# Kernel tuning notes

Measured on AMD Instinct MI355X. Metric: run time of the kernel, lower is better.

## Reference

```python
import jax, jax.numpy as jnp
import numpy as np

B, S, HID = 2, 2048, 4096
H, P, N, G, K = 128, 64, 128, 8, 4      # heads, head_dim, ssm_state, groups, conv kernel
INTER = H * P                           # 8192
CONV_DIM = INTER + 2 * G * N            # 10240
CHUNK = 128
EPS = 1e-5
DT_MIN, DT_MAX = 0.0, 100.0


def setup_inputs() -> dict:
    key = jax.random.key(0)
    ks = jax.random.split(key, 4)
    proj = INTER + CONV_DIM + H
    return {
        "x": jax.random.normal(ks[0], (B, S, HID), jnp.float32),
        "in_proj_w": jax.random.normal(ks[1], (proj, HID), jnp.float32) * 0.02,
        "conv_w": jax.random.normal(ks[2], (CONV_DIM, 1, K), jnp.float32) * 0.2,
        "conv_b": jnp.zeros((CONV_DIM,), jnp.float32),
        "dt_bias": jnp.ones((H,), jnp.float32),
        "A_log": jnp.log(jnp.arange(1, H + 1, dtype=jnp.float32)),
        "D": jnp.ones((H,), jnp.float32),
        "norm_w": jnp.ones((INTER,), jnp.float32),
        "out_proj_w": jax.random.normal(ks[3], (HID, INTER), jnp.float32) * 0.02,
    }


def _segsum(a):
    # a: (..., c) -> (..., c, c); [i, j] = sum_{k=j+1..i} a[k] for i >= j, else -inf
    c = a.shape[-1]
    s = jnp.cumsum(a, axis=-1)
    diff = s[..., :, None] - s[..., None, :]
    mask = jnp.tril(jnp.ones((c, c), dtype=bool))
    return jnp.where(mask, diff, -jnp.inf)


def reference(x, in_proj_w, conv_w, conv_b, dt_bias, A_log, D, norm_w, out_proj_w):
    b, s, _ = x.shape
    proj = jnp.einsum('bsd,ed->bse', x, in_proj_w)
    gate = proj[..., :INTER]
    hBC = proj[..., INTER:INTER + CONV_DIM]
    dt = proj[..., INTER + CONV_DIM:]                       # (b, s, H)

    # depthwise causal conv1d + silu
    xc = jnp.transpose(hBC, (0, 2, 1))                      # (b, conv_dim, s)
    xc = jax.lax.conv_general_dilated(xc, conv_w, (1,), [(K - 1, 0)],
                                      dimension_numbers=('NCH', 'OIH', 'NCH'),
                                      feature_group_count=CONV_DIM)
    xc = xc + conv_b[None, :, None]
    hBC = jax.nn.silu(jnp.transpose(xc, (0, 2, 1)))

    hs = hBC[..., :INTER].reshape(b, s, H, P)
    Bm = hBC[..., INTER:INTER + G * N].reshape(b, s, G, N)
    Cm = hBC[..., INTER + G * N:].reshape(b, s, G, N)

    A = -jnp.exp(A_log)                                     # (H,)
    dt = jnp.clip(jax.nn.softplus(dt + dt_bias), DT_MIN, DT_MAX)

    rep = H // G
    Bh = jnp.repeat(Bm, rep, axis=2)                        # (b, s, H, N)
    Ch = jnp.repeat(Cm, rep, axis=2)

    nc = s // CHUNK
    xch = (hs * dt[..., None]).reshape(b, nc, CHUNK, H, P)  # dt-scaled input, chunked
    Bc = Bh.reshape(b, nc, CHUNK, H, N)
    Cc = Ch.reshape(b, nc, CHUNK, H, N)
    A_dt = (dt * A).reshape(b, nc, CHUNK, H).transpose(0, 3, 1, 2)  # (b, H, nc, c)
    A_cum = jnp.cumsum(A_dt, axis=-1)

    # intra-chunk (diagonal) contribution
    L = jnp.exp(_segsum(A_dt))                              # (b, H, nc, c, c)
    Y_diag = jnp.einsum('bzlhn,bzshn,bhzls,bzshp->bzlhp', Cc, Bc, L, xch)

    # per-chunk final states
    decay_states = jnp.exp(A_cum[..., -1:] - A_cum)         # (b, H, nc, c)
    states = jnp.einsum('bzlhn,bhzl,bzlhp->bzhpn', Bc, decay_states, xch)

    # inter-chunk recurrence (initial state = 0)
    states_p = jnp.concatenate([jnp.zeros_like(states[:, :1]), states], axis=1)  # (b, nc+1, H, P, N)
    A_last = jnp.pad(A_cum[..., -1], ((0, 0), (0, 0), (1, 0)))                   # (b, H, nc+1)
    decay_chunk = jnp.exp(_segsum(A_last))                                        # (b, H, nc+1, nc+1)
    new_states = jnp.einsum('bhzc,bchpn->bzhpn', decay_chunk, states_p)
    prev = new_states[:, :-1]                                # state entering each chunk

    Y_off = jnp.einsum('bzlhn,bzhpn,bhzl->bzlhp', Cc, prev, jnp.exp(A_cum))
    Y = (Y_diag + Y_off).reshape(b, s, H, P) + hs * D[None, None, :, None]
    y = Y.reshape(b, s, INTER)

    # gated grouped RMSNorm (norm_before_gate=False)
    g = y * jax.nn.silu(gate)
    gg = g.reshape(b, s, G, INTER // G)
    var = jnp.mean(gg * gg, axis=-1, keepdims=True)
    gg = gg * jax.lax.rsqrt(var + EPS)
    out = gg.reshape(b, s, INTER) * norm_w

    return jnp.einsum('bsi,oi->bso', out, out_proj_w)
```

## Files before the change

kernel.cpp:

```cpp
#include <hip/hip_runtime.h>
#include <hip/hip_bf16.h>
#include <cstdint>
#include <cstddef>

#define DEVI __device__ __forceinline__

#define BB 2
#define S_LEN 2048
#define HID_DIM 4096
#define NH 128
#define PD 64
#define NS 128
#define NG 8
#define INTER 8192
#define CONVD 10240
#define PROJ 18560
#define PROJP 18688
#define NC 16
#define BS 4096
#define GN 1024

using short8 = __attribute__((ext_vector_type(8))) short;
using short4v = __attribute__((ext_vector_type(4))) short;
using f32x4  = __attribute__((ext_vector_type(4))) float;
using bf16x8 = __attribute__((ext_vector_type(8))) __bf16;

DEVI float bf2f(short u) {
  union { unsigned int i; float f; } v;
  v.i = ((unsigned int)(unsigned short)u) << 16;
  return v.f;
}
DEVI short f2bf(float f) {
  union { float ff; unsigned int i; } v; v.ff = f;
  unsigned int x = v.i;
  return (short)((x + 0x7fffu + ((x >> 16) & 1u)) >> 16);
}
DEVI f32x4 mfma16(short8 a, short8 b, f32x4 c) {
  return __builtin_amdgcn_mfma_f32_16x16x32_bf16(
      __builtin_bit_cast(bf16x8, a), __builtin_bit_cast(bf16x8, b), c, 0, 0, 0);
}
DEVI void gl_lds16(const short* g, short* l) {
  __builtin_amdgcn_global_load_lds(
      (const __attribute__((address_space(1))) void*)g,
      (__attribute__((address_space(3))) void*)l, 16, 0, 0);
}
DEVI float sigmoidf_(float x) { return 1.f / (1.f + __expf(-x)); }

__global__ __launch_bounds__(256) void cvt_f32_bf16_k(const float* __restrict__ in,
                                                      short* __restrict__ out, size_t n) {
  size_t i = ((size_t)blockIdx.x * 256 + threadIdx.x) * 8;
  if (i + 8 > n) return;
  float4 a = *(const float4*)(in + i);
  float4 b = *(const float4*)(in + i + 4);
  short8 o;
  o[0] = f2bf(a.x); o[1] = f2bf(a.y); o[2] = f2bf(a.z); o[3] = f2bf(a.w);
  o[4] = f2bf(b.x); o[5] = f2bf(b.y); o[6] = f2bf(b.z); o[7] = f2bf(b.w);
  *(short8*)(out + i) = o;
}


#define STG(ISB, BUF, KH, TILE) do { \
  const short* _src = (ISB) ? Bt : A; \
  const int _r0 = (ISB) ? n0 : m0; \
  short* _lb = lds_ + ((ISB) ? 32768 : 0) + ((BUF)*2+(KH))*8192; \
  const int _kt = (TILE)*64 + (KH)*32; \
  { int _row = (wid*2)*16 + srow; int _sl = sps ^ ((_row>>1)&3); \
    gl_lds16(_src + (size_t)(_r0+_row)*K + _kt + _sl*8, _lb + (wid*2)*512); } \
  { int _row = (wid*2+1)*16 + srow; int _sl = sps ^ ((_row>>1)&3); \
    gl_lds16(_src + (size_t)(_r0+_row)*K + _kt + _sl*8, _lb + (wid*2+1)*512); } \
} while(0)

#define NOPS ((void)0)
#define VM6 asm volatile("s_waitcnt vmcnt(6)" ::: "memory")
#define VM0 asm volatile("s_waitcnt vmcnt(0)" ::: "memory")

#define PH(BUF, KH, MIH, DOB, STGS, VMW) do { \
  _Pragma("unroll") \
  for (int _m = 0; _m < 4; ++_m) { \
    int _row = wr*128 + ((MIH)*4+_m)*16 + fr; \
    af[_m] = *(const short8*)(lds_ + ((BUF)*2+(KH))*8192 + _row*32 + ((slot ^ ((_row>>1)&3))<<3)); \
  } \
  if (DOB) { \
    _Pragma("unroll") \
    for (int _n = 0; _n < 4; ++_n) { \
      int _row = wc*64 + _n*16 + fr; \
      bf_[_n] = *(const short8*)(lds_ + 32768 + ((BUF)*2+(KH))*8192 + _row*32 + ((slot ^ ((_row>>1)&3))<<3)); \
    } \
  } \
  STGS; VMW; \
  __builtin_amdgcn_s_barrier(); \
  asm volatile("s_waitcnt lgkmcnt(0)" ::: "memory"); \
  __builtin_amdgcn_sched_barrier(0); \
  __builtin_amdgcn_s_setprio(1); \
  _Pragma("unroll") \
  for (int _m = 0; _m < 4; ++_m) \
    _Pragma("unroll") \
    for (int _n = 0; _n < 4; ++_n) \
      acc[(MIH)*4+_m][_n] = mfma16(af[_m], bf_[_n], acc[(MIH)*4+_m][_n]); \
  __builtin_amdgcn_s_setprio(0); \
  __builtin_amdgcn_s_barrier(); \
} while(0)

template<int CB16>
__global__ __launch_bounds__(512, 2) void gemm256_k(const short* __restrict__ A,
                                                    const short* __restrict__ Bt,
                                                    void* __restrict__ Cout,
                                                    int Nstride, int K, int ntn) {
  __shared__ short lds_[65536];
  const int tid = threadIdx.x, wid = tid >> 6, lane = tid & 63;
  const int nwg = gridDim.x, orig = blockIdx.x;
  const int swz = (orig & 7) * (nwg >> 3) + (orig >> 3);
  const int per_group = ntn << 3;
  const int group = swz / per_group;
  const int rem = swz - group * per_group;
  const int m0 = (group * 8 + (rem & 7)) * 256;
  const int n0 = (rem >> 3) * 256;
  const int wr = wid >> 2, wc = wid & 3;
  const int fr = lane & 15, slot = lane >> 4;
  const int srow = lane >> 2, sps = lane & 3;

  f32x4 acc[8][4] = {};
  short8 af[4], bf_[4];
  const int NT = K >> 6;

  STG(1, 0, 0, 0); STG(0, 0, 0, 0); STG(1, 0, 1, 0); STG(0, 0, 1, 0);
  asm volatile("s_waitcnt vmcnt(4)" ::: "memory");
  STG(1, 1, 0, 1); STG(0, 1, 0, 1); STG(1, 1, 1, 1);
  asm volatile("s_waitcnt vmcnt(6)" ::: "memory");
  __builtin_amdgcn_s_barrier();

  for (int i = 0; i < (NT >> 1) - 1; ++i) {
    const int t = 2 * i;
    PH(0, 0, 0, 1, STG(0, 1, 1, t + 1), NOPS);
    PH(0, 0, 1, 0, STG(1, 0, 0, t + 2), NOPS);
    PH(0, 1, 0, 1, STG(0, 0, 0, t + 2), NOPS);
    PH(0, 1, 1, 0, STG(1, 0, 1, t + 2), VM6);
    PH(1, 0, 0, 1, STG(0, 0, 1, t + 2), NOPS);
    PH(1, 0, 1, 0, STG(1, 1, 0, t + 3), NOPS);
    PH(1, 1, 0, 1, STG(0, 1, 0, t + 3), NOPS);
    PH(1, 1, 1, 0, STG(1, 1, 1, t + 3), VM6);
  }
  PH(0, 0, 0, 1, STG(0, 1, 1, NT - 1), NOPS);
  PH(0, 0, 1, 0, NOPS, NOPS);
  PH(0, 1, 0, 1, NOPS, NOPS);
  PH(0, 1, 1, 0, NOPS, VM0);
  PH(1, 0, 0, 1, NOPS, NOPS);
  PH(1, 0, 1, 0, NOPS, NOPS);
  PH(1, 1, 0, 1, NOPS, NOPS);
  PH(1, 1, 1, 0, NOPS, NOPS);

  const int er = (lane >> 4) * 4, ec = lane & 15;
  if (CB16) {
    short* C = (short*)Cout;
#pragma unroll
    for (int mi = 0; mi < 8; ++mi)
#pragma unroll
      for (int j = 0; j < 4; ++j) {
        size_t base = (size_t)(m0 + wr * 128 + mi * 16 + er + j) * Nstride + n0 + wc * 64 + ec;
#pragma unroll
        for (int ni = 0; ni < 4; ++ni) C[base + ni * 16] = f2bf(acc[mi][ni][j]);
      }
  } else {
    float* C = (float*)Cout;
#pragma unroll
    for (int mi = 0; mi < 8; ++mi)
#pragma unroll
      for (int j = 0; j < 4; ++j) {
        size_t base = (size_t)(m0 + wr * 128 + mi * 16 + er + j) * Nstride + n0 + wc * 64 + ec;
#pragma unroll
        for (int ni = 0; ni < 4; ++ni) C[base + ni * 16] = acc[mi][ni][j];
      }
  }
}

__global__ __launch_bounds__(256) void conv_silu_k(const short* __restrict__ projb,
                                                   const float* __restrict__ convw,
                                                   const float* __restrict__ convb,
                                                   short* __restrict__ hbc) {
  const int c = blockIdx.x * 256 + threadIdx.x;
  const int s0 = blockIdx.y * 256;
  const int b = blockIdx.z;
  const size_t rb = (size_t)b * S_LEN;
  const float* wp = convw + (size_t)c * 4;
  const float w0 = wp[0], w1 = wp[1], w2 = wp[2], w3 = wp[3];
  const float bias = convb[c];
  const short* pcol = projb + INTER + c;
  float x1 = 0.f, x2 = 0.f, x3 = 0.f;
  if (s0 > 0) {
    x3 = bf2f(pcol[(rb + s0 - 3) * PROJP]);
    x2 = bf2f(pcol[(rb + s0 - 2) * PROJP]);
    x1 = bf2f(pcol[(rb + s0 - 1) * PROJP]);
  }
  for (int s = s0; s < s0 + 256; ++s) {
    float v = bf2f(pcol[(rb + s) * PROJP]);
    float acc = bias + w0 * x3 + w1 * x2 + w2 * x1 + w3 * v;
    float o = acc * sigmoidf_(acc);
    hbc[(rb + s) * CONVD + c] = f2bf(o);
    x3 = x2; x2 = x1; x1 = v;
  }
}

__global__ __launch_bounds__(128) void acum_k(const short* __restrict__ projb,
                                              const float* __restrict__ dt_bias,
                                              const float* __restrict__ A_log,
                                              float* __restrict__ dtT,
                                              float* __restrict__ acum) {
  const int l = threadIdx.x;
  const int z = blockIdx.x, h = blockIdx.y, b = blockIdx.z;
  const float A = -__expf(A_log[h]);
  __shared__ float sv[128];
  const int r = b * S_LEN + z * 128 + l;
  float xv = bf2f(projb[(size_t)r * PROJP + INTER + CONVD + h]) + dt_bias[h];
  float sp = (xv > 20.f) ? xv : log1pf(__expf(xv));
  sp = fminf(fmaxf(sp, 0.f), 100.f);
  const size_t base = ((size_t)(b * NH + h)) * S_LEN + z * 128;
  dtT[base + l] = sp;
  sv[l] = sp * A;
  __syncthreads();
  for (int off = 1; off < 128; off <<= 1) {
    float t = (l >= off) ? sv[l - off] : 0.f;
    __syncthreads();
    sv[l] += t;
    __syncthreads();
  }
  acum[base + l] = sv[l];
}

__global__ __launch_bounds__(512) void states_k(const short* __restrict__ hbc,
                                                const float* __restrict__ dtT,
                                                const float* __restrict__ acum,
                                                float* __restrict__ states) {
  __shared__ short sB[128 * 128];
  __shared__ short sxdt[64 * 128];
  __shared__ float sac[128];
  const int tid = threadIdx.x, wid = tid >> 6, lane = tid & 63;
  const int g = blockIdx.x, z = blockIdx.y, b = blockIdx.z;
  const size_t srow0 = (size_t)(b * S_LEN + z * 128);
  const short* hrow = hbc + srow0 * CONVD;

  {
    const int n0_ = (lane & 15) * 8;
#pragma unroll
    for (int it = 0; it < 4; ++it) {
      int s = it * 32 + wid * 4 + (lane >> 4);
      gl_lds16(hrow + (size_t)s * CONVD + INTER + g * NS + n0_, sB + (it * 32 + wid * 4) * 128);
    }
  }

  const int fr = lane & 15, fk8 = (lane >> 4) * 8;
  const int er = (lane >> 4) * 4, ec = lane & 15;
  const int nbase = wid * 16;

  for (int hh = 0; hh < 16; ++hh) {
    const int h = g * 16 + hh;
    const float* ac = acum + ((size_t)(b * NH + h)) * S_LEN + z * 128;
    const float* dts = dtT + ((size_t)(b * NH + h)) * S_LEN + z * 128;
    __syncthreads();
    if (tid < 128) sac[tid] = ac[tid];
    {
      int s = tid >> 2, p0 = (tid & 3) * 16;
      float dv = dts[s];
      short8 hv0 = *(const short8*)(hrow + (size_t)s * CONVD + (size_t)h * PD + p0);
      short8 hv1 = *(const short8*)(hrow + (size_t)s * CONVD + (size_t)h * PD + p0 + 8);
#pragma unroll
      for (int j = 0; j < 8; ++j) {
        sxdt[(p0 + j) * 128 + s] = f2bf(bf2f(hv0[j]) * dv);
        sxdt[(p0 + 8 + j) * 128 + s] = f2bf(bf2f(hv1[j]) * dv);
      }
    }
    __syncthreads();
    const float acLast = sac[127];
    f32x4 st[4] = {};
#pragma unroll
    for (int kk = 0; kk < 4; ++kk) {
      short8 a;
#pragma unroll
      for (int j = 0; j < 8; ++j) {
        int l = kk * 32 + fk8 + j;
        float dec = __expf(acLast - sac[l]);
        a[j] = f2bf(bf2f(sB[l * 128 + nbase + fr]) * dec);
      }
#pragma unroll
      for (int ni = 0; ni < 4; ++ni) {
        short8 bv = *(const short8*)(sxdt + (ni * 16 + fr) * 128 + kk * 32 + fk8);
        st[ni] = mfma16(a, bv, st[ni]);
      }
    }
    float* stp = states + (((size_t)(b * NC + z)) * NH + h) * (size_t)(NS * PD);
#pragma unroll
    for (int ni = 0; ni < 4; ++ni)
#pragma unroll
      for (int j = 0; j < 4; ++j)
        stp[(nbase + er + j) * PD + ni * 16 + ec] = st[ni][j];
  }
}

__global__ __launch_bounds__(256) void scan_k(float* __restrict__ states,
                                              const float* __restrict__ acum) {
  const int h = blockIdx.x, b = blockIdx.y;
  const int tid = threadIdx.x;
  float* stp = states + ((size_t)(b * NC * NH) + h) * (size_t)(NS * PD);
  const size_t cst = (size_t)NH * NS * PD;
  const float* ac = acum + ((size_t)(b * NH + h)) * S_LEN;
  float E[32];
#pragma unroll
  for (int i = 0; i < 32; ++i) E[i] = 0.f;
  for (int zz = 0; zz < NC; ++zz) {
    float* sz = stp + (size_t)zz * cst;
    float tmp[32];
#pragma unroll
    for (int i = 0; i < 32; ++i) tmp[i] = sz[i * 256 + tid];
    __syncthreads();
    float dec = __expf(ac[zz * 128 + 127]);
#pragma unroll
    for (int i = 0; i < 32; ++i) {
      int e = i * 256 + tid;
      int n = e >> 6, p = e & 63;
      sz[p * NS + n] = E[i];
      E[i] = dec * E[i] + tmp[i];
    }
    __syncthreads();
  }
}

__global__ __launch_bounds__(512) void yfull_k(const short* __restrict__ hbc,
                                               const short* __restrict__ projb,
                                               const float* __restrict__ dtT,
                                               const float* __restrict__ acum,
                                               const float* __restrict__ states,
                                               const float* __restrict__ Dv,
                                               const float* __restrict__ norm_w,
                                               float* __restrict__ Yg,
                                               short* __restrict__ normed) {
  __shared__ short lds[49152];
  __shared__ float sac[128];
  __shared__ float sScale[128];
  __shared__ float sNW[1024];
  short* sC = lds;
  short* sB = lds + 16384;
  short* sxdt = lds + 16384;
  short* sprev = lds + 16384 + 8192;
  const int tid = threadIdx.x, wid = tid >> 6, lane = tid & 63;
  short* sPw = lds + 32768 + wid * 2048;
  const int g = blockIdx.x, z = blockIdx.y, b = blockIdx.z;
  const size_t srow0 = (size_t)(b * S_LEN + z * 128);
  const short* hrow = hbc + srow0 * CONVD;

  {
    const int n0_ = (lane & 15) * 8;
#pragma unroll
    for (int it = 0; it < 4; ++it) {
      int s = it * 32 + wid * 4 + (lane >> 4);
      gl_lds16(hrow + (size_t)s * CONVD + INTER + GN + g * NS + n0_, sC + (it * 32 + wid * 4) * 128);
      gl_lds16(hrow + (size_t)s * CONVD + INTER + g * NS + n0_, sB + (it * 32 + wid * 4) * 128);
    }
  }
  for (int i = tid; i < 1024; i += 512) sNW[i] = norm_w[g * 1024 + i];
  __syncthreads();

  const int fr = lane & 15, fk8 = (lane >> 4) * 8;
  const int er = (lane >> 4) * 4, ec = lane & 15;
  const int lrow = wid * 16;

  f32x4 sc[8] = {};
#pragma unroll
  for (int kk = 0; kk < 4; ++kk) {
    short8 a = *(const short8*)(sC + (lrow + fr) * 128 + kk * 32 + fk8);
#pragma unroll
    for (int si = 0; si < 8; ++si) {
      short8 bv = *(const short8*)(sB + (si * 16 + fr) * 128 + kk * 32 + fk8);
      sc[si] = mfma16(a, bv, sc[si]);
    }
  }

  float rssq[4] = {0.f, 0.f, 0.f, 0.f};

  for (int hh = 0; hh < 16; ++hh) {
    const int h = g * 16 + hh;
    const float* ac = acum + ((size_t)(b * NH + h)) * S_LEN + z * 128;
    const float* dts = dtT + ((size_t)(b * NH + h)) * S_LEN + z * 128;
    const float* pv = states + (((size_t)(b * NC + z)) * NH + h) * (size_t)(NS * PD);
    __syncthreads();
    if (tid < 128) sac[tid] = ac[tid];
    {
      int s = tid >> 2, p0 = (tid & 3) * 16;
      float dv = dts[s];
      short8 hv0 = *(const short8*)(hrow + (size_t)s * CONVD + (size_t)h * PD + p0);
      short8 hv1 = *(const short8*)(hrow + (size_t)s * CONVD + (size_t)h * PD + p0 + 8);
#pragma unroll
      for (int j = 0; j < 8; ++j) {
        sxdt[(p0 + j) * 128 + s] = f2bf(bf2f(hv0[j]) * dv);
        sxdt[(p0 + 8 + j) * 128 + s] = f2bf(bf2f(hv1[j]) * dv);
      }
    }
#pragma unroll
    for (int it = 0; it < 4; ++it) {
      int e = (it * 512 + tid) * 4;
      float4 v = *(const float4*)(pv + e);
      short4v o;
      o[0] = f2bf(v.x); o[1] = f2bf(v.y); o[2] = f2bf(v.z); o[3] = f2bf(v.w);
      *(short4v*)(sprev + e) = o;
    }
    __syncthreads();

    {
      float acS[8];
#pragma unroll
      for (int si = 0; si < 8; ++si) acS[si] = sac[si * 16 + ec];
#pragma unroll
      for (int j = 0; j < 4; ++j) {
        int lloc = er + j;
        float acl = sac[lrow + lloc];
#pragma unroll
        for (int si = 0; si < 8; ++si) {
          int s = si * 16 + ec;
          float v = (s <= lrow + lloc) ? sc[si][j] * __expf(acl - acS[si]) : 0.f;
          sPw[lloc * 128 + s] = f2bf(v);
        }
      }
    }
    f32x4 yd[4] = {}, yo[4] = {};
#pragma unroll
    for (int kk = 0; kk < 4; ++kk) {
      short8 ap = *(const short8*)(sPw + fr * 128 + kk * 32 + fk8);
      short8 acf = *(const short8*)(sC + (lrow + fr) * 128 + kk * 32 + fk8);
#pragma unroll
      for (int ni = 0; ni < 4; ++ni) {
        short8 bv = *(const short8*)(sxdt + (ni * 16 + fr) * 128 + kk * 32 + fk8);
        yd[ni] = mfma16(ap, bv, yd[ni]);
        short8 bp = *(const short8*)(sprev + (ni * 16 + fr) * 128 + kk * 32 + fk8);
        yo[ni] = mfma16(acf, bp, yo[ni]);
      }
    }
    const float Dh = Dv[h];
#pragma unroll
    for (int j = 0; j < 4; ++j) {
      int l = lrow + er + j;
      float e_ac = __expf(sac[l]);
#pragma unroll
      for (int ni = 0; ni < 4; ++ni) {
        int p = ni * 16 + ec;
        float hs = bf2f(hrow[(size_t)l * CONVD + (size_t)h * PD + p]);
        float y = yd[ni][j] + yo[ni][j] * e_ac + hs * Dh;
        float gate = bf2f(projb[(srow0 + l) * (size_t)PROJP + (size_t)h * PD + p]);
        float gg = y * gate * sigmoidf_(gate);
        Yg[(srow0 + l) * (size_t)INTER + (size_t)h * PD + p] = gg;
        rssq[j] += gg * gg;
      }
    }
  }

#pragma unroll
  for (int j = 0; j < 4; ++j) {
#pragma unroll
    for (int m = 1; m <= 8; m <<= 1) rssq[j] += __shfl_xor(rssq[j], m, 64);
  }
  if (ec == 0) {
#pragma unroll
    for (int j = 0; j < 4; ++j) sScale[lrow + er + j] = rsqrtf(rssq[j] * (1.f / 1024.f) + 1e-5f);
  }
  __syncthreads();

  for (int e = tid * 8; e < 128 * 1024; e += 4096) {
    int row = e >> 10, ch = e & 1023;
    const float* gp = Yg + (srow0 + row) * (size_t)INTER + g * 1024 + ch;
    float4 g0 = *(const float4*)(gp);
    float4 g1 = *(const float4*)(gp + 4);
    float scl = sScale[row];
    short8 o;
    o[0] = f2bf(g0.x * scl * sNW[ch + 0]); o[1] = f2bf(g0.y * scl * sNW[ch + 1]);
    o[2] = f2bf(g0.z * scl * sNW[ch + 2]); o[3] = f2bf(g0.w * scl * sNW[ch + 3]);
    o[4] = f2bf(g1.x * scl * sNW[ch + 4]); o[5] = f2bf(g1.y * scl * sNW[ch + 5]);
    o[6] = f2bf(g1.z * scl * sNW[ch + 6]); o[7] = f2bf(g1.w * scl * sNW[ch + 7]);
    *(short8*)(normed + (srow0 + row) * (size_t)INTER + g * 1024 + ch) = o;
  }
}

extern "C" void kernel_launch(void* const* d_in, const int* in_sizes, int n_in,
                              void* d_out, int out_size, void* d_ws, size_t ws_size,
                              hipStream_t stream) {
  const float* x     = (const float*)d_in[0];
  const float* w1    = (const float*)d_in[1];
  const float* convw = (const float*)d_in[2];
  const float* convb = (const float*)d_in[3];
  const float* dtb   = (const float*)d_in[4];
  const float* alog  = (const float*)d_in[5];
  const float* Dv    = (const float*)d_in[6];
  const float* nw    = (const float*)d_in[7];
  const float* w2    = (const float*)d_in[8];
  float* out = (float*)d_out;

  char* ws = (char*)d_ws;
  size_t off = 0;
  float* dtT = (float*)(ws + off);  off += (size_t)BB * NH * S_LEN * 4;
  float* acum = (float*)(ws + off); off += (size_t)BB * NH * S_LEN * 4;
  short* xb = (short*)(ws + off);   off += (size_t)BS * HID_DIM * 2;
  char* w1region = ws + off;        off += (size_t)PROJP * HID_DIM * 2;
  short* w1b = (short*)w1region;
  short* normed = (short*)w1region;
  short* w2b = (short*)(w1region + (size_t)BS * INTER * 2);
  short* projb = (short*)(ws + off); off += (size_t)BS * PROJP * 2;
  short* hbc = (short*)(ws + off);   off += (size_t)BS * CONVD * 2;
  float* Y = (float*)(ws + off);     off += (size_t)BS * INTER * 4;
  float* states = (float*)(ws + off); off += (size_t)BB * NC * NH * NS * PD * 4;

  const size_t nx = (size_t)BS * HID_DIM;
  const size_t nw1 = (size_t)PROJ * HID_DIM;
  const size_t nw2 = (size_t)HID_DIM * INTER;

  cvt_f32_bf16_k<<<dim3(nx / 2048), 256, 0, stream>>>(x, xb, nx);
  cvt_f32_bf16_k<<<dim3(nw1 / 2048), 256, 0, stream>>>(w1, w1b, nw1);

  gemm256_k<1><<<dim3(16 * 73), 512, 0, stream>>>(xb, w1b, projb, PROJP, HID_DIM, 73);

  cvt_f32_bf16_k<<<dim3(nw2 / 2048), 256, 0, stream>>>(w2, w2b, nw2);

  conv_silu_k<<<dim3(CONVD / 256, S_LEN / 256, BB), 256, 0, stream>>>(projb, convw, convb, hbc);
  acum_k<<<dim3(NC, NH, BB), 128, 0, stream>>>(projb, dtb, alog, dtT, acum);

  states_k<<<dim3(NG, NC, BB), 512, 0, stream>>>(hbc, dtT, acum, states);
  scan_k<<<dim3(NH, BB), 256, 0, stream>>>(states, acum);
  yfull_k<<<dim3(NG, NC, BB), 512, 0, stream>>>(hbc, projb, dtT, acum, states, Dv, nw, Y, normed);

  gemm256_k<0><<<dim3(16 * 16), 512, 0, stream>>>(normed, w2b, out, HID_DIM, INTER, 16);
}
```

Measured before the change: 1.392 ms.

## Restructure SSM state kernels: transposed B tile, bf16 state handoff, padded LDS

Widens the GEMM block swizzle group from 8 to 16 M-tiles to change L2 reuse. The states kernel now folds the decay into the x*dt staging and stores B transposed in LDS, which removes per-element exp and conversion work from the MFMA inner loop. The scan kernel writes the propagated states as bf16 in the layout yfull expects, so yfull can fetch them with direct global-to-LDS loads instead of converting fp32. yfull also packs two bf16 values per 32-bit LDS store and pads its per-wave P rows to reduce bank conflicts. The previous-state operand is now rounded to bf16 in the scan kernel rather than in yfull, and it overwrites the first half of the fp32 state buffer in place.

```diff
diff --git a/kernel.cpp b/kernel.cpp
--- a/kernel.cpp
+++ b/kernel.cpp
@@ -110,11 +110,11 @@
   const int tid = threadIdx.x, wid = tid >> 6, lane = tid & 63;
   const int nwg = gridDim.x, orig = blockIdx.x;
   const int swz = (orig & 7) * (nwg >> 3) + (orig >> 3);
-  const int per_group = ntn << 3;
+  const int per_group = ntn << 4;
   const int group = swz / per_group;
   const int rem = swz - group * per_group;
-  const int m0 = (group * 8 + (rem & 7)) * 256;
-  const int n0 = (rem >> 3) * 256;
+  const int m0 = (group * 16 + (rem & 15)) * 256;
+  const int n0 = (rem >> 4) * 256;
   const int wr = wid >> 2, wc = wid & 3;
   const int fr = lane & 15, slot = lane >> 4;
   const int srow = lane >> 2, sps = lane & 3;
@@ -230,60 +230,63 @@
                                                 const float* __restrict__ dtT,
                                                 const float* __restrict__ acum,
                                                 float* __restrict__ states) {
-  __shared__ short sB[128 * 128];
+  __shared__ short sBT[128 * 128];
   __shared__ short sxdt[64 * 128];
-  __shared__ float sac[128];
   const int tid = threadIdx.x, wid = tid >> 6, lane = tid & 63;
   const int g = blockIdx.x, z = blockIdx.y, b = blockIdx.z;
   const size_t srow0 = (size_t)(b * S_LEN + z * 128);
   const short* hrow = hbc + srow0 * CONVD;
 
   {
-    const int n0_ = (lane & 15) * 8;
-#pragma unroll
-    for (int it = 0; it < 4; ++it) {
-      int s = it * 32 + wid * 4 + (lane >> 4);
-      gl_lds16(hrow + (size_t)s * CONVD + INTER + g * NS + n0_, sB + (it * 32 + wid * 4) * 128);
+    const int l = tid & 127, n0b = (tid >> 7) * 32;
+    const short* src = hrow + (size_t)l * CONVD + INTER + g * NS + n0b;
+    short8 v0 = *(const short8*)(src);
+    short8 v1 = *(const short8*)(src + 8);
+    short8 v2 = *(const short8*)(src + 16);
+    short8 v3 = *(const short8*)(src + 24);
+#pragma unroll
+    for (int j = 0; j < 8; ++j) {
+      sBT[(n0b + j) * 128 + l] = v0[j];
+      sBT[(n0b + 8 + j) * 128 + l] = v1[j];
+      sBT[(n0b + 16 + j) * 128 + l] = v2[j];
+      sBT[(n0b + 24 + j) * 128 + l] = v3[j];
     }
   }
 
   const int fr = lane & 15, fk8 = (lane >> 4) * 8;
   const int er = (lane >> 4) * 4, ec = lane & 15;
-  const int nbase = wid * 16;
+  const int pband = (wid & 3) * 16, nhalf = (wid >> 2) * 64;
+  const int s2 = tid & 63, p0w = (tid >> 6) * 8;
+  unsigned int* sx32 = (unsigned int*)sxdt;
 
   for (int hh = 0; hh < 16; ++hh) {
     const int h = g * 16 + hh;
-    const float* ac = acum + ((size_t)(b * NH + h)) * S_LEN + z * 128;
+    const float* ac_g = acum + ((size_t)(b * NH + h)) * S_LEN + z * 128;
     const float* dts = dtT + ((size_t)(b * NH + h)) * S_LEN + z * 128;
     __syncthreads();
-    if (tid < 128) sac[tid] = ac[tid];
     {
-      int s = tid >> 2, p0 = (tid & 3) * 16;
-      float dv = dts[s];
-      short8 hv0 = *(const short8*)(hrow + (size_t)s * CONVD + (size_t)h * PD + p0);
-      short8 hv1 = *(const short8*)(hrow + (size_t)s * CONVD + (size_t)h * PD + p0 + 8);
+      const float acL = ac_g[127];
+      float dv0 = dts[2 * s2] * __expf(acL - ac_g[2 * s2]);
+      float dv1 = dts[2 * s2 + 1] * __expf(acL - ac_g[2 * s2 + 1]);
+      const short* rsrc = hrow + (size_t)(2 * s2) * CONVD + (size_t)h * PD + p0w;
+      short8 r0 = *(const short8*)(rsrc);
+      short8 r1 = *(const short8*)(rsrc + CONVD);
 #pragma unroll
       for (int j = 0; j < 8; ++j) {
-        sxdt[(p0 + j) * 128 + s] = f2bf(bf2f(hv0[j]) * dv);
-        sxdt[(p0 + 8 + j) * 128 + s] = f2bf(bf2f(hv1[j]) * dv);
-      }
-    }
-    __syncthreads();
-    const float acLast = sac[127];
+        unsigned int lo = (unsigned short)f2bf(bf2f(r0[j]) * dv0);
+        unsigned int hi = (unsigned short)f2bf(bf2f(r1[j]) * dv1);
+        sx32[(p0w + j) * 64 + s2] = lo | (hi << 16);
+      }
+    }
+    __syncthreads();
     f32x4 st[4] = {};
 #pragma unroll
     for (int kk = 0; kk < 4; ++kk) {
-      short8 a;
-#pragma unroll
-      for (int j = 0; j < 8; ++j) {
-        int l = kk * 32 + fk8 + j;
-        float dec = __expf(acLast - sac[l]);
-        a[j] = f2bf(bf2f(sB[l * 128 + nbase + fr]) * dec);
-      }
+      short8 a = *(const short8*)(sxdt + (pband + fr) * 128 + kk * 32 + fk8);
 #pragma unroll
       for (int ni = 0; ni < 4; ++ni) {
-        short8 bv = *(const short8*)(sxdt + (ni * 16 + fr) * 128 + kk * 32 + fk8);
-        st[ni] = mfma16(a, bv, st[ni]);
+        short8 bb = *(const short8*)(sBT + (nhalf + ni * 16 + fr) * 128 + kk * 32 + fk8);
+        st[ni] = mfma16(a, bb, st[ni]);
       }
     }
     float* stp = states + (((size_t)(b * NC + z)) * NH + h) * (size_t)(NS * PD);
@@ -291,7 +294,7 @@
     for (int ni = 0; ni < 4; ++ni)
 #pragma unroll
       for (int j = 0; j < 4; ++j)
-        stp[(nbase + er + j) * PD + ni * 16 + ec] = st[ni][j];
+        stp[(pband + er + j) * NS + nhalf + ni * 16 + ec] = st[ni][j];
   }
 }
 
@@ -305,8 +308,10 @@
   float E[32];
 #pragma unroll
   for (int i = 0; i < 32; ++i) E[i] = 0.f;
+  const int n = tid & 127, pg = tid >> 7;
   for (int zz = 0; zz < NC; ++zz) {
     float* sz = stp + (size_t)zz * cst;
+    short* pvb = (short*)sz;
     float tmp[32];
 #pragma unroll
     for (int i = 0; i < 32; ++i) tmp[i] = sz[i * 256 + tid];
@@ -314,9 +319,8 @@
     float dec = __expf(ac[zz * 128 + 127]);
 #pragma unroll
     for (int i = 0; i < 32; ++i) {
-      int e = i * 256 + tid;
-      int n = e >> 6, p = e & 63;
-      sz[p * NS + n] = E[i];
+      int p = i * 2 + pg;
+      pvb[p * 128 + n] = f2bf(E[i]);
       E[i] = dec * E[i] + tmp[i];
     }
     __syncthreads();
@@ -332,7 +336,7 @@
                                                const float* __restrict__ norm_w,
                                                float* __restrict__ Yg,
                                                short* __restrict__ normed) {
-  __shared__ short lds[49152];
+  __shared__ short lds[50176];
   __shared__ float sac[128];
   __shared__ float sScale[128];
   __shared__ float sNW[1024];
@@ -341,7 +345,7 @@
   short* sxdt = lds + 16384;
   short* sprev = lds + 16384 + 8192;
   const int tid = threadIdx.x, wid = tid >> 6, lane = tid & 63;
-  short* sPw = lds + 32768 + wid * 2048;
+  short* sPw = lds + 32768 + wid * 2176;
   const int g = blockIdx.x, z = blockIdx.y, b = blockIdx.z;
   const size_t srow0 = (size_t)(b * S_LEN + z * 128);
   const short* hrow = hbc + srow0 * CONVD;
@@ -361,6 +365,8 @@
   const int fr = lane & 15, fk8 = (lane >> 4) * 8;
   const int er = (lane >> 4) * 4, ec = lane & 15;
   const int lrow = wid * 16;
+  const int s2 = tid & 63, p0w = (tid >> 6) * 8;
+  unsigned int* sx32 = (unsigned int*)sxdt;
 
   f32x4 sc[8] = {};
 #pragma unroll
@@ -379,28 +385,23 @@
     const int h = g * 16 + hh;
     const float* ac = acum + ((size_t)(b * NH + h)) * S_LEN + z * 128;
     const float* dts = dtT + ((size_t)(b * NH + h)) * S_LEN + z * 128;
-    const float* pv = states + (((size_t)(b * NC + z)) * NH + h) * (size_t)(NS * PD);
+    const short* pvb = (const short*)(states + (((size_t)(b * NC + z)) * NH + h) * (size_t)(NS * PD));
     __syncthreads();
     if (tid < 128) sac[tid] = ac[tid];
     {
-      int s = tid >> 2, p0 = (tid & 3) * 16;
-      float dv = dts[s];
-      short8 hv0 = *(const short8*)(hrow + (size_t)s * CONVD + (size_t)h * PD + p0);
-      short8 hv1 = *(const short8*)(hrow + (size_t)s * CONVD + (size_t)h * PD + p0 + 8);
+      float dv0 = dts[2 * s2], dv1 = dts[2 * s2 + 1];
+      const short* rsrc = hrow + (size_t)(2 * s2) * CONVD + (size_t)h * PD + p0w;
+      short8 r0 = *(const short8*)(rsrc);
+      short8 r1 = *(const short8*)(rsrc + CONVD);
 #pragma unroll
       for (int j = 0; j < 8; ++j) {
-        sxdt[(p0 + j) * 128 + s] = f2bf(bf2f(hv0[j]) * dv);
-        sxdt[(p0 + 8 + j) * 128 + s] = f2bf(bf2f(hv1[j]) * dv);
-      }
-    }
-#pragma unroll
-    for (int it = 0; it < 4; ++it) {
-      int e = (it * 512 + tid) * 4;
-      float4 v = *(const float4*)(pv + e);
-      short4v o;
-      o[0] = f2bf(v.x); o[1] = f2bf(v.y); o[2] = f2bf(v.z); o[3] = f2bf(v.w);
-      *(short4v*)(sprev + e) = o;
-    }
+        unsigned int lo = (unsigned short)f2bf(bf2f(r0[j]) * dv0);
+        unsigned int hi = (unsigned short)f2bf(bf2f(r1[j]) * dv1);
+        sx32[(p0w + j) * 64 + s2] = lo | (hi << 16);
+      }
+    }
+    gl_lds16(pvb + wid * 1024 + lane * 8, sprev + wid * 1024);
+    gl_lds16(pvb + wid * 1024 + 512 + lane * 8, sprev + wid * 1024 + 512);
     __syncthreads();
 
     {
@@ -415,14 +416,14 @@
         for (int si = 0; si < 8; ++si) {
           int s = si * 16 + ec;
           float v = (s <= lrow + lloc) ? sc[si][j] * __expf(acl - acS[si]) : 0.f;
-          sPw[lloc * 128 + s] = f2bf(v);
+          sPw[lloc * 136 + s] = f2bf(v);
         }
       }
     }
     f32x4 yd[4] = {}, yo[4] = {};
 #pragma unroll
     for (int kk = 0; kk < 4; ++kk) {
-      short8 ap = *(const short8*)(sPw + fr * 128 + kk * 32 + fk8);
+      short8 ap = *(const short8*)(sPw + fr * 136 + kk * 32 + fk8);
       short8 acf = *(const short8*)(sC + (lrow + fr) * 128 + kk * 32 + fk8);
 #pragma unroll
       for (int ni = 0; ni < 4; ++ni) {
```

New measurement: 1.286 ms. 1.08x faster.
